# Performance work log

Measured on AMD Instinct MI355X. Metric: run time of the kernel, lower is better.

Reference implementation:

```python
import jax, jax.numpy as jnp
import numpy as np

N = 8          # codebooks per embedding
N_E = 1024     # codebook size
E_DIM = 64     # codebook dim
BETA = 0.25
GAMMA = 1.0


def setup_inputs() -> dict:
    key = jax.random.key(0)
    k1, k2 = jax.random.split(key)
    z = jax.random.normal(k1, (8192, N * E_DIM), dtype=jnp.float32)
    # nn.Embedding weight init: uniform(-1/n_e, 1/n_e)
    emb_weight = jax.random.uniform(k2, (N_E, E_DIM), dtype=jnp.float32,
                                    minval=-1.0 / N_E, maxval=1.0 / N_E)
    return {"z": z, "emb_weight": emb_weight}


def reference(z, emb_weight):
    B = z.shape[0]
    zr = z.reshape(B, N, E_DIM)                 # (B, n, e_dim)
    z_flat = zr.reshape(-1, E_DIM)              # (B*n, e_dim)

    # squared L2 distance to every codebook entry: (B*n, n_e)
    d = (jnp.sum(z_flat ** 2, axis=1, keepdims=True)
         + jnp.sum(emb_weight ** 2, axis=1)
         - 2.0 * z_flat @ emb_weight.T)

    min_encoding_indices = jnp.argmin(d, axis=1)[:, None]          # (B*n, 1)
    min_encodings = jax.nn.one_hot(min_encoding_indices[:, 0], N_E,
                                   dtype=z.dtype)                  # (B*n, n_e)

    z_q = (min_encodings @ emb_weight).reshape(zr.shape)           # (B, n, e_dim)

    loss1 = jnp.mean((jax.lax.stop_gradient(z_q) - zr) ** 2)
    loss2 = jnp.mean((z_q - jax.lax.stop_gradient(zr)) ** 2)
    loss = GAMMA * loss1 + BETA * loss2

    # straight-through estimator
    z_q_st = zr + jax.lax.stop_gradient(z_q - zr)

    e_mean = jnp.mean(min_encodings, axis=0)
    perplexity = jnp.exp(-jnp.sum(e_mean * jnp.log(e_mean + 1e-10)))

    z_output = z_q_st.reshape(B, -1)
    return (loss, loss1, loss2, z_q_st, z_output, perplexity,
            min_encodings, min_encoding_indices)
```

## Files before the change

kernel.cpp:

```cpp
#include <hip/hip_runtime.h>
#include <math.h>

#define DIM 64
#define NCODES 1024
#define NROWS 65536

#define OFF_ZQ   3L
#define OFF_ZOUT 4194307L
#define OFF_PERP 8388611L
#define OFF_ENC  8388612L
#define OFF_IDX  75497476L

#define MARGIN 1e-4f

typedef __attribute__((ext_vector_type(8))) short short8;
typedef __attribute__((ext_vector_type(4))) float f32x4;

static __device__ __forceinline__ unsigned short f2bf_rne(float x) {
    unsigned u = __float_as_uint(x);
    return (unsigned short)((u + 0x7fffu + ((u >> 16) & 1u)) >> 16);
}

__global__ __launch_bounds__(256) void k_prep(const float* __restrict__ emb,
                                              float* __restrict__ E_np,
                                              short* __restrict__ Bp,
                                              float* __restrict__ embT,
                                              unsigned int* __restrict__ hist,
                                              double* __restrict__ lossAcc,
                                              unsigned int* __restrict__ ambCount)
{
    const int j = blockIdx.x * 4 + (threadIdx.x >> 6);
    const int d = threadIdx.x & 63;

    float e = emb[j * DIM + d];
    float s = e * e;
    asm volatile("" : "+v"(s));

    float rr[8];
    #pragma unroll
    for (int t = 0; t < 8; ++t) rr[t] = __shfl(s, t, 64);
    #pragma unroll
    for (int i = 1; i < 8; ++i)
        #pragma unroll
        for (int t = 0; t < 8; ++t) rr[t] += __shfl(s, 8 * i + t, 64);
    float En = ((rr[0] + rr[1]) + (rr[2] + rr[3])) + ((rr[4] + rr[5]) + (rr[6] + rr[7]));
    if (d == 0) E_np[j] = En;
    if (d == 1) hist[j] = 0u;

    unsigned short h = f2bf_rne(e);
    float hf = __uint_as_float(((unsigned)h) << 16);
    unsigned short lo = f2bf_rne(e - hf);

    const int t = j >> 4, c = j & 15;
    int pos;
    if (d < 32) pos = t * 2048 + ((d >> 3) * 16 + c) * 8 + (d & 7);
    else        pos = t * 2048 + 512 + (((d - 32) >> 3) * 16 + c) * 8 + ((d - 32) & 7);
    Bp[pos] = (short)h;
    Bp[pos + 1024] = (short)lo;

    embT[d * 1024 + j] = e;

    if (blockIdx.x == 0 && threadIdx.x == 0) { *lossAcc = 0.0; *ambCount = 0u; }
}

__global__ __launch_bounds__(256) void k_main(const float* __restrict__ z,
                                              const short* __restrict__ Bp,
                                              const float* __restrict__ E_np,
                                              int* __restrict__ idx,
                                              unsigned int* __restrict__ ambCount,
                                              unsigned int* __restrict__ ambList)
{
    const int lane = threadIdx.x & 63;
    const int l15 = lane & 15;
    const int lHi = lane >> 4;
    const int waveRow = (threadIdx.x >> 6) * 32;
    const long rowBase = (long)blockIdx.x * 128 + waveRow;

    short8 ah[4], al[4];
    #pragma unroll
    for (int t = 0; t < 2; ++t) {
        #pragma unroll
        for (int c = 0; c < 2; ++c) {
            const float* zp = z + (rowBase + t * 16 + l15) * DIM + c * 32 + lHi * 8;
            float4 v0 = *(const float4*)zp;
            float4 v1 = *(const float4*)(zp + 4);
            float xs[8] = {v0.x, v0.y, v0.z, v0.w, v1.x, v1.y, v1.z, v1.w};
            short8 hi, lo;
            #pragma unroll
            for (int e = 0; e < 8; ++e) {
                unsigned short h = f2bf_rne(xs[e]);
                float hf = __uint_as_float(((unsigned)h) << 16);
                hi[e] = (short)h;
                lo[e] = (short)f2bf_rne(xs[e] - hf);
            }
            ah[t * 2 + c] = hi;
            al[t * 2 + c] = lo;
        }
    }

    float b1v[8], b2v[8];
    int b1j[8];
    #pragma unroll
    for (int s = 0; s < 8; ++s) { b1v[s] = INFINITY; b2v[s] = INFINITY; b1j[s] = 0; }

    #pragma unroll 1
    for (int tt = 0; tt < 64; ++tt) {
        const int code = tt * 16 + l15;
        const float e2 = E_np[code];
        const short* base = Bp + (size_t)tt * 2048;
        short8 beh0 = *(const short8*)(base + lane * 8);
        short8 beh1 = *(const short8*)(base + 512 + lane * 8);
        short8 bel0 = *(const short8*)(base + 1024 + lane * 8);
        short8 bel1 = *(const short8*)(base + 1536 + lane * 8);

        #pragma unroll
        for (int t = 0; t < 2; ++t) {
            f32x4 zz = {0.f, 0.f, 0.f, 0.f};
            f32x4 p = __builtin_amdgcn_mfma_f32_16x16x32_bf16(ah[2 * t + 0], beh0, zz, 0, 0, 0);
            p = __builtin_amdgcn_mfma_f32_16x16x32_bf16(al[2 * t + 0], beh0, p, 0, 0, 0);
            p = __builtin_amdgcn_mfma_f32_16x16x32_bf16(ah[2 * t + 0], bel0, p, 0, 0, 0);
            f32x4 q = __builtin_amdgcn_mfma_f32_16x16x32_bf16(ah[2 * t + 1], beh1, zz, 0, 0, 0);
            q = __builtin_amdgcn_mfma_f32_16x16x32_bf16(al[2 * t + 1], beh1, q, 0, 0, 0);
            q = __builtin_amdgcn_mfma_f32_16x16x32_bf16(ah[2 * t + 1], bel1, q, 0, 0, 0);

            #pragma unroll
            for (int r = 0; r < 4; ++r) {
                float dist = fmaf(-2.f, p[r] + q[r], e2);
                int s = t * 4 + r;
                bool lt1 = dist < b1v[s];
                float nb2 = lt1 ? b1v[s] : fminf(b2v[s], dist);
                b1j[s] = lt1 ? code : b1j[s];
                b1v[s] = lt1 ? dist : b1v[s];
                b2v[s] = nb2;
            }
        }
    }

    #pragma unroll
    for (int s = 0; s < 8; ++s) {
        float v1 = b1v[s], v2 = b2v[s];
        int j1 = b1j[s];
        #pragma unroll
        for (int off = 8; off > 0; off >>= 1) {
            float o1 = __shfl_xor(v1, off, 16);
            float o2 = __shfl_xor(v2, off, 16);
            int   oj = __shfl_xor(j1, off, 16);
            bool take = (o1 < v1);
            float n2 = take ? fminf(v1, o2) : fminf(o1, v2);
            if (take) { v1 = o1; j1 = oj; }
            v2 = n2;
        }
        if (l15 == 0) {
            long row = rowBase + (s >> 2) * 16 + lHi * 4 + (s & 3);
            idx[row] = j1;
            if (v2 - v1 < MARGIN) {
                unsigned int ppos = atomicAdd(ambCount, 1u);
                ambList[ppos] = (unsigned int)row;
            }
        }
    }
}

__global__ __launch_bounds__(256) void k_recheck(const float* __restrict__ z,
                                                 const float* __restrict__ embT,
                                                 const float* __restrict__ E_np,
                                                 int* __restrict__ idx,
                                                 const unsigned int* __restrict__ ambCount,
                                                 const unsigned int* __restrict__ ambList)
{
    const int lane = threadIdx.x & 63;
    const unsigned gwave = blockIdx.x * 4 + (threadIdx.x >> 6);
    const unsigned nwaves = gridDim.x * 4;
    const unsigned cnt = *ambCount;
    const unsigned ngroups = (cnt + 3) >> 2;

    for (unsigned w = gwave; w < ngroups; w += nwaves) {
        int rows[4];
        #pragma unroll
        for (int i = 0; i < 4; ++i) {
            unsigned p = w * 4 + (unsigned)i;
            rows[i] = (int)ambList[p < cnt ? p : w * 4];
        }

        float a2v[4], Zfv[4];
        #pragma unroll
        for (int i = 0; i < 4; ++i) {
            float zl = z[(long)rows[i] * DIM + lane];
            float z2 = zl * zl;
            a2v[i] = 2.f * zl;
            float rr[8];
            #pragma unroll
            for (int t = 0; t < 8; ++t) rr[t] = __shfl(z2, t, 64);
            #pragma unroll
            for (int t = 1; t < 8; ++t)
                #pragma unroll
                for (int u = 0; u < 8; ++u) rr[u] += __shfl(z2, 8 * t + u, 64);
            Zfv[i] = ((rr[0] + rr[1]) + (rr[2] + rr[3])) + ((rr[4] + rr[5]) + (rr[6] + rr[7]));
        }

        float acc[4][4][4];
        #pragma unroll
        for (int i = 0; i < 4; ++i)
            #pragma unroll
            for (int c = 0; c < 4; ++c)
                #pragma unroll
                for (int m = 0; m < 4; ++m) acc[i][c][m] = 0.f;

        #pragma unroll 1
        for (int dq = 0; dq < 16; ++dq) {
            float b[4][4];
            #pragma unroll
            for (int i = 0; i < 4; ++i)
                #pragma unroll
                for (int kk = 0; kk < 4; ++kk)
                    b[i][kk] = __shfl(a2v[i], 4 * dq + kk, 64);
            #pragma unroll
            for (int c = 0; c < 4; ++c) {
                #pragma unroll
                for (int kk = 0; kk < 4; ++kk) {
                    const f32x4 e4 = *(const f32x4*)(embT + (4 * dq + kk) * 1024 + 4 * lane + 256 * c);
                    #pragma unroll
                    for (int i = 0; i < 4; ++i)
                        #pragma unroll
                        for (int m = 0; m < 4; ++m)
                            acc[i][c][m] = fmaf(b[i][kk], e4[m], acc[i][c][m]);
                }
            }
        }

        float bv[4];
        int bj[4];
        #pragma unroll
        for (int i = 0; i < 4; ++i) { bv[i] = INFINITY; bj[i] = 1 << 29; }

        #pragma unroll
        for (int c = 0; c < 4; ++c) {
            const f32x4 En4 = *(const f32x4*)(E_np + 4 * lane + 256 * c);
            #pragma unroll
            for (int m = 0; m < 4; ++m) {
                int j = 4 * lane + 256 * c + m;
                #pragma unroll
                for (int i = 0; i < 4; ++i) {
                    float dd = (Zfv[i] + En4[m]) - acc[i][c][m];
                    if (dd < bv[i] || (dd == bv[i] && j < bj[i])) { bv[i] = dd; bj[i] = j; }
                }
            }
        }

        #pragma unroll
        for (int i = 0; i < 4; ++i) {
            float v = bv[i];
            int j = bj[i];
            #pragma unroll
            for (int off = 32; off > 0; off >>= 1) {
                float ov = __shfl_xor(v, off, 64);
                int   oj = __shfl_xor(j, off, 64);
                if (ov < v || (ov == v && oj < j)) { v = ov; j = oj; }
            }
            if (lane == 0) idx[rows[i]] = j;
        }
    }
}

__global__ __launch_bounds__(256) void k_out(const float* __restrict__ z,
                                             const float* __restrict__ emb,
                                             const int* __restrict__ idx,
                                             float* __restrict__ out,
                                             unsigned int* __restrict__ hist,
                                             double* __restrict__ lossAcc)
{
    f32x4* out_enc = (f32x4*)(out + OFF_ENC);
    const long totalA = (long)NROWS * (NCODES / 4);
    for (long v = (long)blockIdx.x * 256 + threadIdx.x; v < totalA;
         v += (long)gridDim.x * 256) {
        int r = (int)(v >> 8);
        int j0 = ((int)v & 255) * 4;
        int i = idx[r];
        f32x4 o;
        o.x = (j0 == i)     ? 1.f : 0.f;
        o.y = (j0 + 1 == i) ? 1.f : 0.f;
        o.z = (j0 + 2 == i) ? 1.f : 0.f;
        o.w = (j0 + 3 == i) ? 1.f : 0.f;
        __builtin_nontemporal_store(o, out_enc + v);
    }

    __shared__ double red[256];
    double part = 0.0;
    const long totalB = (long)NROWS * (DIM / 4);
    for (long g4 = (long)blockIdx.x * 256 + threadIdx.x; g4 < totalB;
         g4 += (long)gridDim.x * 256) {
        int r = (int)(g4 >> 4);
        int d0 = ((int)g4 & 15) * 4;
        int i = idx[r];
        float4 e = *(const float4*)(emb + i * DIM + d0);
        float4 zv = *(const float4*)(z + g4 * 4);
        float tx = e.x - zv.x, ty = e.y - zv.y, tz = e.z - zv.z, tw = e.w - zv.w;
        f32x4 zq = {zv.x + tx, zv.y + ty, zv.z + tz, zv.w + tw};
        __builtin_nontemporal_store(zq, (f32x4*)(out + OFF_ZQ + g4 * 4));
        __builtin_nontemporal_store(zq, (f32x4*)(out + OFF_ZOUT + g4 * 4));
        part = fma((double)tx, (double)tx, part);
        part = fma((double)ty, (double)ty, part);
        part = fma((double)tz, (double)tz, part);
        part = fma((double)tw, (double)tw, part);
        if (d0 == 0) {
            atomicAdd(&hist[i], 1u);
            out[OFF_IDX + r] = (float)i;
        }
    }
    red[threadIdx.x] = part;
    __syncthreads();
    for (int s = 128; s > 0; s >>= 1) {
        if (threadIdx.x < s) red[threadIdx.x] += red[threadIdx.x + s];
        __syncthreads();
    }
    if (threadIdx.x == 0) atomicAdd(lossAcc, red[0]);
}

__global__ __launch_bounds__(256) void k_final(const unsigned int* __restrict__ hist,
                                               const double* __restrict__ lossAcc,
                                               float* __restrict__ out)
{
    __shared__ double red[256];
    double part = 0.0;
    for (int b = threadIdx.x; b < NCODES; b += 256) {
        double em = (double)hist[b] * (1.0 / 65536.0);
        part += em * log(em + 1e-10);
    }
    red[threadIdx.x] = part;
    __syncthreads();
    for (int s = 128; s > 0; s >>= 1) {
        if (threadIdx.x < s) red[threadIdx.x] += red[threadIdx.x + s];
        __syncthreads();
    }
    if (threadIdx.x == 0) {
        double H = -red[0];
        double perp = exp(H);
        double m = *lossAcc * (1.0 / 4194304.0);
        out[0] = (float)(m + 0.25 * m);
        out[1] = (float)m;
        out[2] = (float)m;
        out[OFF_PERP] = (float)perp;
    }
}

extern "C" void kernel_launch(void* const* d_in, const int* in_sizes, int n_in,
                              void* d_out, int out_size, void* d_ws, size_t ws_size,
                              hipStream_t stream)
{
    const float* z   = (const float*)d_in[0];
    const float* emb = (const float*)d_in[1];
    float* out = (float*)d_out;
    char* ws = (char*)d_ws;

    int*          idx      = (int*)(ws + 0);
    unsigned int* hist     = (unsigned int*)(ws + 262144);
    double*       lossAcc  = (double*)(ws + 266240);
    float*        E_np     = (float*)(ws + 266752);
    unsigned int* ambCount = (unsigned int*)(ws + 270848);
    unsigned int* ambList  = (unsigned int*)(ws + 270852);

    float* scratch = out + OFF_ENC;
    short* Bp   = (short*)scratch;
    float* embT = scratch + 65536;

    hipLaunchKernelGGL(k_prep,    dim3(256),  dim3(256), 0, stream, emb, E_np, Bp, embT, hist, lossAcc, ambCount);
    hipLaunchKernelGGL(k_main,    dim3(512),  dim3(256), 0, stream, z, Bp, E_np, idx, ambCount, ambList);
    hipLaunchKernelGGL(k_recheck, dim3(256),  dim3(256), 0, stream, z, embT, E_np, idx, ambCount, ambList);
    hipLaunchKernelGGL(k_out,     dim3(2048), dim3(256), 0, stream, z, emb, idx, out, hist, lossAcc);
    hipLaunchKernelGGL(k_final,   dim3(1),    dim3(256), 0, stream, hist, lossAcc, out);
}
```

Measured before the change: 214.0 us.

## Overlap one-hot zero fill with GEMM blocks and fuse finalize into output kernel

```diff
diff --git a/kernel.cpp b/kernel.cpp
--- a/kernel.cpp
+++ b/kernel.cpp
@@ -12,6 +12,10 @@
 #define OFF_IDX  75497476L
 
 #define MARGIN 1e-4f
+
+#define GEMM_BLOCKS 512
+#define FILL_BLOCKS 2048
+#define OUT_BLOCKS  1024
 
 typedef __attribute__((ext_vector_type(8))) short short8;
 typedef __attribute__((ext_vector_type(4))) float f32x4;
@@ -27,7 +31,8 @@
                                               float* __restrict__ embT,
                                               unsigned int* __restrict__ hist,
                                               double* __restrict__ lossAcc,
-                                              unsigned int* __restrict__ ambCount)
+                                              unsigned int* __restrict__ ambCount,
+                                              unsigned int* __restrict__ doneCnt)
 {
     const int j = blockIdx.x * 4 + (threadIdx.x >> 6);
     const int d = threadIdx.x & 63;
@@ -60,7 +65,11 @@
 
     embT[d * 1024 + j] = e;
 
-    if (blockIdx.x == 0 && threadIdx.x == 0) { *lossAcc = 0.0; *ambCount = 0u; }
+    if (blockIdx.x == 0 && threadIdx.x == 0) {
+        *lossAcc = 0.0;
+        *ambCount = 0u;
+        *doneCnt = 0u;
+    }
 }
 
 __global__ __launch_bounds__(256) void k_main(const float* __restrict__ z,
@@ -68,8 +77,20 @@
                                               const float* __restrict__ E_np,
                                               int* __restrict__ idx,
                                               unsigned int* __restrict__ ambCount,
-                                              unsigned int* __restrict__ ambList)
-{
+                                              unsigned int* __restrict__ ambList,
+                                              float* __restrict__ out)
+{
+    if (blockIdx.x >= GEMM_BLOCKS) {
+        f32x4* enc = (f32x4*)(out + OFF_ENC);
+        const long totalA = (long)NROWS * (NCODES / 4);
+        const f32x4 zero = {0.f, 0.f, 0.f, 0.f};
+        long v = (long)(blockIdx.x - GEMM_BLOCKS) * 256 + threadIdx.x;
+        const long stride = (long)FILL_BLOCKS * 256;
+        for (; v < totalA; v += stride)
+            __builtin_nontemporal_store(zero, enc + v);
+        return;
+    }
+
     const int lane = threadIdx.x & 63;
     const int l15 = lane & 15;
     const int lHi = lane >> 4;
@@ -267,24 +288,11 @@
                                              const int* __restrict__ idx,
                                              float* __restrict__ out,
                                              unsigned int* __restrict__ hist,
-                                             double* __restrict__ lossAcc)
-{
-    f32x4* out_enc = (f32x4*)(out + OFF_ENC);
-    const long totalA = (long)NROWS * (NCODES / 4);
-    for (long v = (long)blockIdx.x * 256 + threadIdx.x; v < totalA;
-         v += (long)gridDim.x * 256) {
-        int r = (int)(v >> 8);
-        int j0 = ((int)v & 255) * 4;
-        int i = idx[r];
-        f32x4 o;
-        o.x = (j0 == i)     ? 1.f : 0.f;
-        o.y = (j0 + 1 == i) ? 1.f : 0.f;
-        o.z = (j0 + 2 == i) ? 1.f : 0.f;
-        o.w = (j0 + 3 == i) ? 1.f : 0.f;
-        __builtin_nontemporal_store(o, out_enc + v);
-    }
-
+                                             double* __restrict__ lossAcc,
+                                             unsigned int* __restrict__ doneCnt)
+{
     __shared__ double red[256];
+    __shared__ int lastFlag;
     double part = 0.0;
     const long totalB = (long)NROWS * (DIM / 4);
     for (long g4 = (long)blockIdx.x * 256 + threadIdx.x; g4 < totalB;
@@ -305,6 +313,7 @@
         if (d0 == 0) {
             atomicAdd(&hist[i], 1u);
             out[OFF_IDX + r] = (float)i;
+            out[OFF_ENC + (long)r * NCODES + i] = 1.0f;
         }
     }
     red[threadIdx.x] = part;
@@ -313,33 +322,35 @@
         if (threadIdx.x < s) red[threadIdx.x] += red[threadIdx.x + s];
         __syncthreads();
     }
-    if (threadIdx.x == 0) atomicAdd(lossAcc, red[0]);
-}
-
-__global__ __launch_bounds__(256) void k_final(const unsigned int* __restrict__ hist,
-                                               const double* __restrict__ lossAcc,
-                                               float* __restrict__ out)
-{
-    __shared__ double red[256];
-    double part = 0.0;
-    for (int b = threadIdx.x; b < NCODES; b += 256) {
-        double em = (double)hist[b] * (1.0 / 65536.0);
-        part += em * log(em + 1e-10);
-    }
-    red[threadIdx.x] = part;
+    if (threadIdx.x == 0) {
+        atomicAdd(lossAcc, red[0]);
+        __threadfence();
+        unsigned v = atomicAdd(doneCnt, 1u);
+        lastFlag = (v == (unsigned)(gridDim.x - 1)) ? 1 : 0;
+    }
     __syncthreads();
-    for (int s = 128; s > 0; s >>= 1) {
-        if (threadIdx.x < s) red[threadIdx.x] += red[threadIdx.x + s];
+    if (lastFlag) {
+        __threadfence();
+        double p2 = 0.0;
+        for (int b = threadIdx.x; b < NCODES; b += 256) {
+            double em = (double)hist[b] * (1.0 / 65536.0);
+            p2 += em * log(em + 1e-10);
+        }
+        red[threadIdx.x] = p2;
         __syncthreads();
-    }
-    if (threadIdx.x == 0) {
-        double H = -red[0];
-        double perp = exp(H);
-        double m = *lossAcc * (1.0 / 4194304.0);
-        out[0] = (float)(m + 0.25 * m);
-        out[1] = (float)m;
-        out[2] = (float)m;
-        out[OFF_PERP] = (float)perp;
+        for (int s = 128; s > 0; s >>= 1) {
+            if (threadIdx.x < s) red[threadIdx.x] += red[threadIdx.x + s];
+            __syncthreads();
+        }
+        if (threadIdx.x == 0) {
+            double H = -red[0];
+            double perp = exp(H);
+            double m = *lossAcc * (1.0 / 4194304.0);
+            out[0] = (float)(m + 0.25 * m);
+            out[1] = (float)m;
+            out[2] = (float)m;
+            out[OFF_PERP] = (float)perp;
+        }
     }
 }
 
@@ -358,14 +369,14 @@
     float*        E_np     = (float*)(ws + 266752);
     unsigned int* ambCount = (unsigned int*)(ws + 270848);
     unsigned int* ambList  = (unsigned int*)(ws + 270852);
-
-    float* scratch = out + OFF_ENC;
+    unsigned int* doneCnt  = (unsigned int*)(ws + 532996);
+
+    float* scratch = out + OFF_ZQ + 1;
     short* Bp   = (short*)scratch;
     float* embT = scratch + 65536;
 
-    hipLaunchKernelGGL(k_prep,    dim3(256),  dim3(256), 0, stream, emb, E_np, Bp, embT, hist, lossAcc, ambCount);
-    hipLaunchKernelGGL(k_main,    dim3(512),  dim3(256), 0, stream, z, Bp, E_np, idx, ambCount, ambList);
-    hipLaunchKernelGGL(k_recheck, dim3(256),  dim3(256), 0, stream, z, embT, E_np, idx, ambCount, ambList);
-    hipLaunchKernelGGL(k_out,     dim3(2048), dim3(256), 0, stream, z, emb, idx, out, hist, lossAcc);
-    hipLaunchKernelGGL(k_final,   dim3(1),    dim3(256), 0, stream, hist, lossAcc, out);
-}
+    hipLaunchKernelGGL(k_prep,    dim3(256),                      dim3(256), 0, stream, emb, E_np, Bp, embT, hist, lossAcc, ambCount, doneCnt);
+    hipLaunchKernelGGL(k_main,    dim3(GEMM_BLOCKS + FILL_BLOCKS), dim3(256), 0, stream, z, Bp, E_np, idx, ambCount, ambList, out);
+    hipLaunchKernelGGL(k_recheck, dim3(256),                      dim3(256), 0, stream, z, embT, E_np, idx, ambCount, ambList);
+    hipLaunchKernelGGL(k_out,     dim3(OUT_BLOCKS),               dim3(256), 0, stream, z, emb, idx, out, hist, lossAcc, doneCnt);
+}
```

Result: slower. 258.9 us (+21.0%).
